# Kernel optimization log

Hardware: AMD Instinct MI355X
Metric: run time of the kernel (lower is better)

Reference implementation:

```python
import jax, jax.numpy as jnp
import numpy as np

B = 131072
INPUT_SIZE = 128
HIDDEN_SIZE = 128


def setup_inputs() -> dict:
    key = jax.random.key(0)
    ks = jax.random.split(key, 11)
    stdv = 1.0 / (HIDDEN_SIZE ** 0.5)

    def unif(k, shape):
        return jax.random.uniform(k, shape, dtype=jnp.float32, minval=-stdv, maxval=stdv)

    return {
        "x_t": jax.random.normal(ks[0], (B, INPUT_SIZE), dtype=jnp.float32),
        "h_prev": jax.random.normal(ks[1], (B, HIDDEN_SIZE), dtype=jnp.float32),
        "Wz": unif(ks[2], (INPUT_SIZE, HIDDEN_SIZE)),
        "Uz": unif(ks[3], (HIDDEN_SIZE, HIDDEN_SIZE)),
        "bz": unif(ks[4], (HIDDEN_SIZE,)),
        "Wr": unif(ks[5], (INPUT_SIZE, HIDDEN_SIZE)),
        "Ur": unif(ks[6], (HIDDEN_SIZE, HIDDEN_SIZE)),
        "br": unif(ks[7], (HIDDEN_SIZE,)),
        "Wh": unif(ks[8], (INPUT_SIZE, HIDDEN_SIZE)),
        "Uh": unif(ks[9], (HIDDEN_SIZE, HIDDEN_SIZE)),
        "bh": unif(ks[10], (HIDDEN_SIZE,)),
    }


def reference(x_t, h_prev, Wz, Uz, bz, Wr, Ur, br, Wh, Uh, bh):
    # Fuse the three input-side and two hidden-side GEMMs by concatenating weights.
    W = jnp.concatenate([Wz, Wr, Wh], axis=1)        # [I, 3H]
    U = jnp.concatenate([Uz, Ur], axis=1)            # [H, 2H]
    xw = x_t @ W                                     # [B, 3H]
    hu = h_prev @ U                                  # [B, 2H]
    H = bz.shape[0]
    z_t = jax.nn.sigmoid(xw[:, :H] + hu[:, :H] + bz)
    r_t = jax.nn.sigmoid(xw[:, H:2 * H] + hu[:, H:] + br)
    h_cand = jnp.tanh(xw[:, 2 * H:] + (r_t * h_prev) @ Uh + bh)
    h_t = (1.0 - z_t) * h_prev + z_t * h_cand
    return h_t
```

## Files before the change

### kernel.cpp

```cpp
#include <hip/hip_runtime.h>
#include <hip/hip_bf16.h>

typedef __attribute__((ext_vector_type(8))) short bf16x8;
typedef __attribute__((ext_vector_type(4))) float f32x4;

#define GRU_B 131072
#define BM 32
#define TPB 4
#define NBLK (GRU_B / (BM * TPB))

static __device__ __forceinline__ ushort f2bf(float f) {
  union { float f; unsigned u; } v; v.f = f;
  unsigned r = v.u + 0x7FFFu + ((v.u >> 16) & 1u);
  return (ushort)(r >> 16);
}
static __device__ __forceinline__ float bf2f(ushort u) {
  union { unsigned u; float f; } v; v.u = ((unsigned)u) << 16;
  return v.f;
}
static __device__ __forceinline__ unsigned pk2(float a, float b) {
  float2 t; t.x = a; t.y = b;
  __hip_bfloat162 r = __float22bfloat162_rn(t);
  union { __hip_bfloat162 b; unsigned u; } cv; cv.b = r;
  return cv.u;
}
static __device__ __forceinline__ float fsig(float x) {
  return __builtin_amdgcn_rcpf(1.0f + __expf(-x));
}
static __device__ __forceinline__ float ftanh(float x) {
  return 1.0f - 2.0f * __builtin_amdgcn_rcpf(1.0f + __expf(2.0f * x));
}
static __device__ __forceinline__ int swz(int row, int cbyte) {
  return (row * 256 + cbyte) ^ ((row & 7) << 4) ^ ((row & 8) << 2);
}

#define BARRIER() do {                                       \
  asm volatile("s_waitcnt lgkmcnt(0)" ::: "memory");         \
  __builtin_amdgcn_s_barrier();                              \
  asm volatile("" ::: "memory");                             \
} while (0)

__global__ void wtrans_kernel(const float* __restrict__ wz, const float* __restrict__ uz,
                              const float* __restrict__ wr, const float* __restrict__ ur,
                              const float* __restrict__ wh, const float* __restrict__ uh,
                              ushort* __restrict__ outw) {
  int f = blockIdx.x * 256 + threadIdx.x;
  int mat = f >> 14;
  int rem = f & 16383;
  int chunk = rem >> 9;
  int lane = (rem >> 3) & 63;
  int e = rem & 7;
  int cb = chunk >> 2, k0b = chunk & 3;
  int n = cb * 16 + (lane & 15);
  int k = k0b * 32 + (lane >> 4) * 8 + e;
  const float* src = (mat == 0) ? wz : (mat == 1) ? uz : (mat == 2) ? wr
                   : (mat == 3) ? ur : (mat == 4) ? wh : uh;
  outw[f] = f2bf(src[k * 128 + n]);
}

#define MFMA __builtin_amdgcn_mfma_f32_16x16x32_bf16

__global__ __launch_bounds__(512, 2) void gru_kernel(
    const float* __restrict__ x, const float* __restrict__ hprev,
    const ushort* __restrict__ wt,
    const float* __restrict__ bz, const float* __restrict__ br,
    const float* __restrict__ bh, float* __restrict__ out) {
  __shared__ __align__(16) char smem[49152];

  const int tid = threadIdx.x;
  const int lane = tid & 63;
  const int wid = tid >> 6;
  const int l15 = lane & 15;
  const int q = lane >> 4;
  const int n0 = wid * 16;

  const float4 brv = *(const float4*)(br + n0 + q * 4);
  const float4 bzv = *(const float4*)(bz + n0 + q * 4);
  const float4 bhv = *(const float4*)(bh + n0 + q * 4);
  const f32x4 brv4 = {brv.x, brv.y, brv.z, brv.w};
  const f32x4 bzv4 = {bzv.x, bzv.y, bzv.z, bzv.w};
  const f32x4 bhv4 = {bhv.x, bhv.y, bhv.z, bhv.w};

  const ushort* wlane = wt + (lane << 3);
  auto wfrag = [&](int mat, int kb) -> const bf16x8* {
    return (const bf16x8*)(wlane + ((((mat << 3) + wid) << 2) + kb) * 512);
  };

  auto ldsA = [&](const char* base, int mr, int k0) -> bf16x8 {
    int row = mr * 16 + l15;
    return *(const bf16x8*)(base + swz(row, (k0 + q * 8) * 2));
  };

  const long tile0 = (long)blockIdx.x * TPB;
  const float4* xg = (const float4*)x;
  const float4* hg = (const float4*)hprev;

  const int r0 = tid >> 5, cb0 = (tid & 31) << 3;
  const int bo0 = swz(r0, cb0), bo1 = swz(r0 + 16, cb0);
  const int go0 = swz(l15, (n0 + q * 4) * 2);
  const int go1 = swz(16 + l15, (n0 + q * 4) * 2);

  auto stage = [&](char* S, const float4& a0, const float4& a1,
                   const float4& b0, const float4& b1) {
    uint2 v;
    v.x = pk2(a0.x, a0.y); v.y = pk2(a0.z, a0.w); *(uint2*)(S + bo0) = v;
    v.x = pk2(a1.x, a1.y); v.y = pk2(a1.z, a1.w); *(uint2*)(S + bo1) = v;
    v.x = pk2(b0.x, b0.y); v.y = pk2(b0.z, b0.w); *(uint2*)(S + 8192 + bo0) = v;
    v.x = pk2(b1.x, b1.y); v.y = pk2(b1.z, b1.w); *(uint2*)(S + 8192 + bo1) = v;
  };

  float4 px0, px1, ph0, ph1;
  {
    long toff = tile0 * 1024;
    px0 = xg[toff + tid]; px1 = xg[toff + 512 + tid];
    ph0 = hg[toff + tid]; ph1 = hg[toff + 512 + tid];
    stage(smem, px0, px1, ph0, ph1);
    if (TPB > 1) {
      toff += 1024;
      px0 = xg[toff + tid]; px1 = xg[toff + 512 + tid];
      ph0 = hg[toff + tid]; ph1 = hg[toff + 512 + tid];
    }
  }
  BARRIER();

  for (int t = 0; t < TPB; ++t) {
    char* Scur = smem + (t & 1) * 16384;
    char* RHc  = smem + 32768 + (t & 1) * 8192;
    const long row0 = (tile0 + t) * BM;

    if (t + 1 < TPB) stage(smem + ((t + 1) & 1) * 16384, px0, px1, ph0, ph1);

    if (t + 2 < TPB) {
      long toff = (tile0 + t + 2) * 1024;
      px0 = xg[toff + tid]; px1 = xg[toff + 512 + tid];
      ph0 = hg[toff + tid]; ph1 = hg[toff + 512 + tid];
    }

    f32x4 accr[2], accz[2], acch[2];
    accr[0] = brv4; accr[1] = brv4;
    accz[0] = bzv4; accz[1] = bzv4;
    acch[0] = bhv4; acch[1] = bhv4;
    __builtin_amdgcn_s_setprio(1);
#pragma unroll
    for (int kb = 0; kb < 4; ++kb) {
      bf16x8 bWz = *wfrag(0, kb);
      bf16x8 bUz = *wfrag(1, kb);
      bf16x8 bWr = *wfrag(2, kb);
      bf16x8 bUr = *wfrag(3, kb);
      bf16x8 bWh = *wfrag(4, kb);
#pragma unroll
      for (int mr = 0; mr < 2; ++mr) {
        bf16x8 ax = ldsA(Scur, mr, kb * 32);
        bf16x8 ah = ldsA(Scur + 8192, mr, kb * 32);
        accr[mr] = MFMA(bWr, ax, accr[mr], 0, 0, 0);
        accr[mr] = MFMA(bUr, ah, accr[mr], 0, 0, 0);
        accz[mr] = MFMA(bWz, ax, accz[mr], 0, 0, 0);
        accz[mr] = MFMA(bUz, ah, accz[mr], 0, 0, 0);
        acch[mr] = MFMA(bWh, ax, acch[mr], 0, 0, 0);
      }
    }
    __builtin_amdgcn_s_setprio(0);

    uint2 hpk[2];
#pragma unroll
    for (int mr = 0; mr < 2; ++mr) {
      int go = mr ? go1 : go0;
      uint2 hp4 = *(const uint2*)(Scur + 8192 + go);
      hpk[mr] = hp4;
      float h0 = bf2f((ushort)(hp4.x & 0xffff)), h1 = bf2f((ushort)(hp4.x >> 16));
      float h2 = bf2f((ushort)(hp4.y & 0xffff)), h3 = bf2f((ushort)(hp4.y >> 16));
      uint2 w;
      w.x = pk2(fsig(accr[mr][0]) * h0, fsig(accr[mr][1]) * h1);
      w.y = pk2(fsig(accr[mr][2]) * h2, fsig(accr[mr][3]) * h3);
      *(uint2*)(RHc + go) = w;
    }

    BARRIER();

    __builtin_amdgcn_s_setprio(1);
#pragma unroll
    for (int kb = 0; kb < 4; ++kb) {
      bf16x8 bUh = *wfrag(5, kb);
#pragma unroll
      for (int mr = 0; mr < 2; ++mr)
        acch[mr] = MFMA(bUh, ldsA(RHc, mr, kb * 32), acch[mr], 0, 0, 0);
    }
    __builtin_amdgcn_s_setprio(0);

#pragma unroll
    for (int mr = 0; mr < 2; ++mr) {
      float hpf[4];
      hpf[0] = bf2f((ushort)(hpk[mr].x & 0xffff));
      hpf[1] = bf2f((ushort)(hpk[mr].x >> 16));
      hpf[2] = bf2f((ushort)(hpk[mr].y & 0xffff));
      hpf[3] = bf2f((ushort)(hpk[mr].y >> 16));
      float4 v;
#pragma unroll
      for (int j = 0; j < 4; ++j) {
        float hc = ftanh(acch[mr][j]);
        float zv = fsig(accz[mr][j]);
        ((float*)&v)[j] = hpf[j] + zv * (hc - hpf[j]);
      }
      *(float4*)(out + (row0 + mr * 16 + l15) * 128 + n0 + q * 4) = v;
    }
  }
}

extern "C" void kernel_launch(void* const* d_in, const int* in_sizes, int n_in,
                              void* d_out, int out_size, void* d_ws, size_t ws_size,
                              hipStream_t stream) {
  const float* x  = (const float*)d_in[0];
  const float* h  = (const float*)d_in[1];
  const float* Wz = (const float*)d_in[2];
  const float* Uz = (const float*)d_in[3];
  const float* bz = (const float*)d_in[4];
  const float* Wr = (const float*)d_in[5];
  const float* Ur = (const float*)d_in[6];
  const float* br = (const float*)d_in[7];
  const float* Wh = (const float*)d_in[8];
  const float* Uh = (const float*)d_in[9];
  const float* bh = (const float*)d_in[10];
  ushort* wt = (ushort*)d_ws;

  hipLaunchKernelGGL(wtrans_kernel, dim3(384), dim3(256), 0, stream,
                     Wz, Uz, Wr, Ur, Wh, Uh, wt);
  hipLaunchKernelGGL(gru_kernel, dim3(NBLK), dim3(512), 0, stream,
                     x, h, wt, bz, br, bh, (float*)d_out);
}
```

Before: 62.83 us.

## Software-pipeline GRU tiles so Uh GEMM overlaps next tile's gate GEMMs

Restructures the per-tile loop into a skewed pipeline. The r·h @ Uh MFMAs for tile t are interleaved with the gate MFMAs for tile t+1, which removes the mid-tile barrier between the r phase and the Uh phase. The change uses triple-buffered input staging with a 64KB LDS footprint and raises tiles per block from 4 to 8, halving the grid. The cost is more registers (two sets of accumulators live at once) and more LDS, which can reduce occupancy below 2 blocks per CU.

```diff
diff --git a/kernel.cpp b/kernel.cpp
--- a/kernel.cpp
+++ b/kernel.cpp
@@ -6,7 +6,7 @@
 
 #define GRU_B 131072
 #define BM 32
-#define TPB 4
+#define TPB 8
 #define NBLK (GRU_B / (BM * TPB))
 
 static __device__ __forceinline__ ushort f2bf(float f) {
@@ -65,7 +65,7 @@
     const ushort* __restrict__ wt,
     const float* __restrict__ bz, const float* __restrict__ br,
     const float* __restrict__ bh, float* __restrict__ out) {
-  __shared__ __align__(16) char smem[49152];
+  __shared__ __align__(16) char smem[65536];
 
   const int tid = threadIdx.x;
   const int lane = tid & 63;
@@ -85,7 +85,6 @@
   auto wfrag = [&](int mat, int kb) -> const bf16x8* {
     return (const bf16x8*)(wlane + ((((mat << 3) + wid) << 2) + kb) * 512);
   };
-
   auto ldsA = [&](const char* base, int mr, int k0) -> bf16x8 {
     int row = mr * 16 + l15;
     return *(const bf16x8*)(base + swz(row, (k0 + q * 8) * 2));
@@ -108,6 +107,20 @@
     v.x = pk2(b0.x, b0.y); v.y = pk2(b0.z, b0.w); *(uint2*)(S + 8192 + bo0) = v;
     v.x = pk2(b1.x, b1.y); v.y = pk2(b1.z, b1.w); *(uint2*)(S + 8192 + bo1) = v;
   };
+  auto rhphase = [&](const char* S, char* RH, const f32x4* accr, uint2* hpk) {
+#pragma unroll
+    for (int mr = 0; mr < 2; ++mr) {
+      int go = mr ? go1 : go0;
+      uint2 hp4 = *(const uint2*)(S + 8192 + go);
+      hpk[mr] = hp4;
+      float h0 = bf2f((ushort)(hp4.x & 0xffff)), h1 = bf2f((ushort)(hp4.x >> 16));
+      float h2 = bf2f((ushort)(hp4.y & 0xffff)), h3 = bf2f((ushort)(hp4.y >> 16));
+      uint2 w;
+      w.x = pk2(fsig(accr[mr][0]) * h0, fsig(accr[mr][1]) * h1);
+      w.y = pk2(fsig(accr[mr][2]) * h2, fsig(accr[mr][3]) * h3);
+      *(uint2*)(RH + go) = w;
+    }
+  };
 
   float4 px0, px1, ph0, ph1;
   {
@@ -115,7 +128,11 @@
     px0 = xg[toff + tid]; px1 = xg[toff + 512 + tid];
     ph0 = hg[toff + tid]; ph1 = hg[toff + 512 + tid];
     stage(smem, px0, px1, ph0, ph1);
-    if (TPB > 1) {
+    toff += 1024;
+    px0 = xg[toff + tid]; px1 = xg[toff + 512 + tid];
+    ph0 = hg[toff + tid]; ph1 = hg[toff + 512 + tid];
+    stage(smem + 16384, px0, px1, ph0, ph1);
+    if (TPB > 2) {
       toff += 1024;
       px0 = xg[toff + tid]; px1 = xg[toff + 512 + tid];
       ph0 = hg[toff + tid]; ph1 = hg[toff + 512 + tid];
@@ -123,85 +140,118 @@
   }
   BARRIER();
 
+  f32x4 aPz[2], aPh[2];
+  uint2 hpkP[2];
+  {
+    f32x4 ar_[2] = {brv4, brv4}, az_[2] = {bzv4, bzv4}, ah_[2] = {bhv4, bhv4};
+#pragma unroll
+    for (int kb = 0; kb < 4; ++kb) {
+      bf16x8 bWz = *wfrag(0, kb), bUz = *wfrag(1, kb);
+      bf16x8 bWr = *wfrag(2, kb), bUr = *wfrag(3, kb);
+      bf16x8 bWh = *wfrag(4, kb);
+#pragma unroll
+      for (int mr = 0; mr < 2; ++mr) {
+        bf16x8 ax = ldsA(smem, mr, kb * 32);
+        bf16x8 ah = ldsA(smem + 8192, mr, kb * 32);
+        ar_[mr] = MFMA(bWr, ax, ar_[mr], 0, 0, 0);
+        ar_[mr] = MFMA(bUr, ah, ar_[mr], 0, 0, 0);
+        az_[mr] = MFMA(bWz, ax, az_[mr], 0, 0, 0);
+        az_[mr] = MFMA(bUz, ah, az_[mr], 0, 0, 0);
+        ah_[mr] = MFMA(bWh, ax, ah_[mr], 0, 0, 0);
+      }
+    }
+    rhphase(smem, smem + 49152, ar_, hpkP);
+    aPz[0] = az_[0]; aPz[1] = az_[1];
+    aPh[0] = ah_[0]; aPh[1] = ah_[1];
+  }
+
   for (int t = 0; t < TPB; ++t) {
-    char* Scur = smem + (t & 1) * 16384;
-    char* RHc  = smem + 32768 + (t & 1) * 8192;
+    BARRIER();
+    char* RHcur = smem + 49152 + (t & 1) * 8192;
     const long row0 = (tile0 + t) * BM;
 
-    if (t + 1 < TPB) stage(smem + ((t + 1) & 1) * 16384, px0, px1, ph0, ph1);
-
-    if (t + 2 < TPB) {
-      long toff = (tile0 + t + 2) * 1024;
-      px0 = xg[toff + tid]; px1 = xg[toff + 512 + tid];
-      ph0 = hg[toff + tid]; ph1 = hg[toff + 512 + tid];
-    }
-
-    f32x4 accr[2], accz[2], acch[2];
-    accr[0] = brv4; accr[1] = brv4;
-    accz[0] = bzv4; accz[1] = bzv4;
-    acch[0] = bhv4; acch[1] = bhv4;
-    __builtin_amdgcn_s_setprio(1);
-#pragma unroll
-    for (int kb = 0; kb < 4; ++kb) {
-      bf16x8 bWz = *wfrag(0, kb);
-      bf16x8 bUz = *wfrag(1, kb);
-      bf16x8 bWr = *wfrag(2, kb);
-      bf16x8 bUr = *wfrag(3, kb);
-      bf16x8 bWh = *wfrag(4, kb);
+    if (t + 1 < TPB) {
+      char* Snx = smem + ((t + 1) % 3) * 16384;
+      f32x4 aNr[2] = {brv4, brv4}, aNz[2] = {bzv4, bzv4}, aNh[2] = {bhv4, bhv4};
+      __builtin_amdgcn_s_setprio(1);
+#pragma unroll
+      for (int kb = 0; kb < 4; ++kb) {
+        bf16x8 bWz = *wfrag(0, kb), bUz = *wfrag(1, kb);
+        bf16x8 bWr = *wfrag(2, kb), bUr = *wfrag(3, kb);
+        bf16x8 bWh = *wfrag(4, kb), bUh = *wfrag(5, kb);
+#pragma unroll
+        for (int mr = 0; mr < 2; ++mr) {
+          bf16x8 ax = ldsA(Snx, mr, kb * 32);
+          bf16x8 ah = ldsA(Snx + 8192, mr, kb * 32);
+          bf16x8 ar = ldsA(RHcur, mr, kb * 32);
+          aPh[mr] = MFMA(bUh, ar, aPh[mr], 0, 0, 0);
+          aNr[mr] = MFMA(bWr, ax, aNr[mr], 0, 0, 0);
+          aNr[mr] = MFMA(bUr, ah, aNr[mr], 0, 0, 0);
+          aNz[mr] = MFMA(bWz, ax, aNz[mr], 0, 0, 0);
+          aNz[mr] = MFMA(bUz, ah, aNz[mr], 0, 0, 0);
+          aNh[mr] = MFMA(bWh, ax, aNh[mr], 0, 0, 0);
+        }
+      }
+      __builtin_amdgcn_s_setprio(0);
+
+      uint2 hpkN[2];
+      rhphase(Snx, smem + 49152 + ((t + 1) & 1) * 8192, aNr, hpkN);
+
+      if (t + 2 < TPB) {
+        stage(smem + ((t + 2) % 3) * 16384, px0, px1, ph0, ph1);
+        if (t + 3 < TPB) {
+          long toff = (tile0 + t + 3) * 1024;
+          px0 = xg[toff + tid]; px1 = xg[toff + 512 + tid];
+          ph0 = hg[toff + tid]; ph1 = hg[toff + 512 + tid];
+        }
+      }
+
 #pragma unroll
       for (int mr = 0; mr < 2; ++mr) {
-        bf16x8 ax = ldsA(Scur, mr, kb * 32);
-        bf16x8 ah = ldsA(Scur + 8192, mr, kb * 32);
-        accr[mr] = MFMA(bWr, ax, accr[mr], 0, 0, 0);
-        accr[mr] = MFMA(bUr, ah, accr[mr], 0, 0, 0);
-        accz[mr] = MFMA(bWz, ax, accz[mr], 0, 0, 0);
-        accz[mr] = MFMA(bUz, ah, accz[mr], 0, 0, 0);
-        acch[mr] = MFMA(bWh, ax, acch[mr], 0, 0, 0);
-      }
-    }
-    __builtin_amdgcn_s_setprio(0);
-
-    uint2 hpk[2];
-#pragma unroll
-    for (int mr = 0; mr < 2; ++mr) {
-      int go = mr ? go1 : go0;
-      uint2 hp4 = *(const uint2*)(Scur + 8192 + go);
-      hpk[mr] = hp4;
-      float h0 = bf2f((ushort)(hp4.x & 0xffff)), h1 = bf2f((ushort)(hp4.x >> 16));
-      float h2 = bf2f((ushort)(hp4.y & 0xffff)), h3 = bf2f((ushort)(hp4.y >> 16));
-      uint2 w;
-      w.x = pk2(fsig(accr[mr][0]) * h0, fsig(accr[mr][1]) * h1);
-      w.y = pk2(fsig(accr[mr][2]) * h2, fsig(accr[mr][3]) * h3);
-      *(uint2*)(RHc + go) = w;
-    }
-
-    BARRIER();
-
-    __builtin_amdgcn_s_setprio(1);
-#pragma unroll
-    for (int kb = 0; kb < 4; ++kb) {
-      bf16x8 bUh = *wfrag(5, kb);
-#pragma unroll
-      for (int mr = 0; mr < 2; ++mr)
-        acch[mr] = MFMA(bUh, ldsA(RHc, mr, kb * 32), acch[mr], 0, 0, 0);
-    }
-    __builtin_amdgcn_s_setprio(0);
-
-#pragma unroll
-    for (int mr = 0; mr < 2; ++mr) {
-      float hpf[4];
-      hpf[0] = bf2f((ushort)(hpk[mr].x & 0xffff));
-      hpf[1] = bf2f((ushort)(hpk[mr].x >> 16));
-      hpf[2] = bf2f((ushort)(hpk[mr].y & 0xffff));
-      hpf[3] = bf2f((ushort)(hpk[mr].y >> 16));
-      float4 v;
-#pragma unroll
-      for (int j = 0; j < 4; ++j) {
-        float hc = ftanh(acch[mr][j]);
-        float zv = fsig(accz[mr][j]);
-        ((float*)&v)[j] = hpf[j] + zv * (hc - hpf[j]);
-      }
-      *(float4*)(out + (row0 + mr * 16 + l15) * 128 + n0 + q * 4) = v;
+        float hpf[4];
+        hpf[0] = bf2f((ushort)(hpkP[mr].x & 0xffff));
+        hpf[1] = bf2f((ushort)(hpkP[mr].x >> 16));
+        hpf[2] = bf2f((ushort)(hpkP[mr].y & 0xffff));
+        hpf[3] = bf2f((ushort)(hpkP[mr].y >> 16));
+        float4 v;
+#pragma unroll
+        for (int j = 0; j < 4; ++j) {
+          float hc = ftanh(aPh[mr][j]);
+          float zv = fsig(aPz[mr][j]);
+          ((float*)&v)[j] = hpf[j] + zv * (hc - hpf[j]);
+        }
+        *(float4*)(out + (row0 + mr * 16 + l15) * 128 + n0 + q * 4) = v;
+      }
+
+      aPz[0] = aNz[0]; aPz[1] = aNz[1];
+      aPh[0] = aNh[0]; aPh[1] = aNh[1];
+      hpkP[0] = hpkN[0]; hpkP[1] = hpkN[1];
+    } else {
+      __builtin_amdgcn_s_setprio(1);
+#pragma unroll
+      for (int kb = 0; kb < 4; ++kb) {
+        bf16x8 bUh = *wfrag(5, kb);
+#pragma unroll
+        for (int mr = 0; mr < 2; ++mr)
+          aPh[mr] = MFMA(bUh, ldsA(RHcur, mr, kb * 32), aPh[mr], 0, 0, 0);
+      }
+      __builtin_amdgcn_s_setprio(0);
+#pragma unroll
+      for (int mr = 0; mr < 2; ++mr) {
+        float hpf[4];
+        hpf[0] = bf2f((ushort)(hpkP[mr].x & 0xffff));
+        hpf[1] = bf2f((ushort)(hpkP[mr].x >> 16));
+        hpf[2] = bf2f((ushort)(hpkP[mr].y & 0xffff));
+        hpf[3] = bf2f((ushort)(hpkP[mr].y >> 16));
+        float4 v;
+#pragma unroll
+        for (int j = 0; j < 4; ++j) {
+          float hc = ftanh(aPh[mr][j]);
+          float zv = fsig(aPz[mr][j]);
+          ((float*)&v)[j] = hpf[j] + zv * (hc - hpf[j]);
+        }
+        *(float4*)(out + (row0 + mr * 16 + l15) * 128 + n0 + q * 4) = v;
+      }
     }
   }
 }
```

Result: slower. 73.72 us (+17.3%).
